# Performance work log

Measured on AMD Instinct MI355X. Metric: run time of the kernel, lower is better.

The kernel has to match this reference:

```python
import jax, jax.numpy as jnp
import numpy as np

B, N, F, FS, OUT, S, H, K = 1024, 256, 64, 128, 128, 4, 4, 4
EPS = 1e-5   # BatchNorm1d eps
BIG = 1e9    # sentinel distance for invalid nodes

# fully-connected segment edges (S nodes per graph, B graphs, flat node indexing)
_base = np.array([(i, j) for i in range(S) for j in range(S) if i != j], dtype=np.int32).T
_offs = (np.arange(B, dtype=np.int32) * S)[:, None]
CSRC = jnp.asarray((_base[0][None, :] + _offs).reshape(-1))
CDST = jnp.asarray((_base[1][None, :] + _offs).reshape(-1))
CMASK = jnp.ones(CSRC.shape[0], jnp.float32)


def _bn_relu(h, gamma, beta):
    # BatchNorm1d in training mode: biased batch statistics over the node axis
    mu = h.mean(0)
    var = jnp.var(h, axis=0)
    return jax.nn.relu((h - mu) * jax.lax.rsqrt(var + EPS) * gamma + beta)


def _graph_conv(x, src, dst, emask, W, b, gamma, beta):
    # linear -> gather(src) -> scatter-add(dst) -> degree norm -> BN -> ReLU
    h = x @ W + b
    agg = jax.ops.segment_sum(h[src] * emask[:, None], dst, num_segments=x.shape[0])
    deg = jnp.clip(jax.ops.segment_sum(emask, dst, num_segments=x.shape[0]), 1.0, None)
    return _bn_relu(h + agg / deg[:, None], gamma, beta)


def _knn_edges(positions, presence):
    # edges (i -> j) for each valid node i to its K nearest valid neighbors j
    valid = presence > 0.5                                    # [B,N]
    n_valid = valid.sum(-1)                                   # [B]
    diff = positions[:, :, None, :] - positions[:, None, :, :]
    d2 = jax.lax.stop_gradient(jnp.sum(diff * diff, -1))      # squared dist, same ordering as cdist
    d2 = jnp.where(valid[:, None, :], d2, BIG)                # mask invalid columns
    negv, idx = jax.lax.top_k(-d2, K + 1)                     # nearest first; idx[...,0] is self (dist 0)
    nbr, nd = idx[:, :, 1:], -negv[:, :, 1:]                  # [B,N,K]
    emask = valid[:, :, None] & (n_valid[:, None, None] >= 2) & (nd < 0.5 * BIG)
    offs = (jnp.arange(B) * N)[:, None, None]
    src = jnp.broadcast_to(jnp.arange(N)[None, :, None] + offs, (B, N, K)).reshape(-1)
    dst = jnp.where(emask, nbr + offs, 0).reshape(-1)
    return src, dst, emask.reshape(-1).astype(jnp.float32)


def setup_inputs() -> dict:
    key = jax.random.key(0)
    ks = jax.random.split(key, 16)
    rn = lambda k, shp, s=0.05: jax.random.normal(k, shp, jnp.float32) * s
    return {
        "axle_features": jax.random.normal(ks[0], (B, N, F), jnp.float32),
        "axle_positions": jax.random.normal(ks[1], (B, N, 2), jnp.float32),
        "presence_scores": jax.random.uniform(ks[2], (B, N), jnp.float32),
        "seg_queries": jax.random.normal(ks[3], (S, F), jnp.float32),
        "wq": rn(ks[4], (F, F)), "bq": jnp.zeros((F,), jnp.float32),
        "wk": rn(ks[5], (F, F)), "bk": jnp.zeros((F,), jnp.float32),
        "w_a2s": rn(ks[6], (F, FS)), "b_a2s": jnp.zeros((FS,), jnp.float32),
        "w_s2a": rn(ks[7], (FS, F)), "b_s2a": jnp.zeros((F,), jnp.float32),
        "coarse_W": rn(ks[8], (2, FS, FS)), "coarse_b": jnp.zeros((2, FS), jnp.float32),
        "coarse_gamma": jnp.ones((2, FS), jnp.float32), "coarse_beta": jnp.zeros((2, FS), jnp.float32),
        "fine_W": rn(ks[9], (3, F, F)), "fine_b": jnp.zeros((3, F), jnp.float32),
        "fine_gamma": jnp.ones((3, F), jnp.float32), "fine_beta": jnp.zeros((3, F), jnp.float32),
        "w_out": rn(ks[10], (F, OUT)), "b_out": jnp.zeros((OUT,), jnp.float32),
    }


def reference(axle_features, axle_positions, presence_scores, seg_queries, wq, bq, wk, bk,
              w_a2s, b_a2s, w_s2a, b_s2a, coarse_W, coarse_b, coarse_gamma, coarse_beta,
              fine_W, fine_b, fine_gamma, fine_beta, w_out, b_out):
    hd = F // H
    # LearnableSegmentation: MHA attention weights (head-averaged), then softmax over segments
    q = (seg_queries @ wq + bq).reshape(S, H, hd)
    k = (axle_features @ wk + bk).reshape(B, N, H, hd)
    scores = jnp.einsum('shd,bnhd->bhsn', q, k) / np.sqrt(hd)
    attn = jax.nn.softmax(scores, -1).mean(1)                 # [B,S,N]
    assign = jax.nn.softmax(jnp.swapaxes(attn, 1, 2), -1)     # [B,N,S]
    # segment pooling + coarse GNN over fully-connected segment graph
    proj = axle_features @ w_a2s + b_a2s                      # [B,N,FS]
    sf = jnp.einsum('bns,bnf->bsf', assign, proj).reshape(B * S, FS)
    for l in range(coarse_W.shape[0]):
        sf = _graph_conv(sf, CSRC, CDST, CMASK, coarse_W[l], coarse_b[l], coarse_gamma[l], coarse_beta[l])
    ctx = jnp.einsum('bns,bsf->bnf', assign, sf.reshape(B, S, FS)) @ w_s2a + b_s2a
    # fine GNN over kNN axle graph
    src, dst, em = _knn_edges(axle_positions, presence_scores)
    af = (axle_features + ctx).reshape(B * N, F)
    for l in range(fine_W.shape[0]):
        af = _graph_conv(af, src, dst, em, fine_W[l], fine_b[l], fine_gamma[l], fine_beta[l])
    # presence-weighted pooling + output projection
    pw = presence_scores[:, :, None]
    g = (af.reshape(B, N, F) * pw).sum(1) / jnp.clip(pw.sum(1), 1e-8, None)
    return g @ w_out + b_out
```

## Files before the change

### kernel.cpp

```cpp
#include <hip/hip_runtime.h>
#include <hip/hip_bf16.h>
#include <math.h>

#define BB   1024
#define NN   256
#define FF   64
#define FSS  128
#define OUTT 128
#define SS   4
#define HH   4
#define KK   4
#define HDD  16
#define EPSF 1e-5f
#define BIGF 1000000000.0f
#define ROWB 72
#define ROWA 68

typedef __attribute__((ext_vector_type(8))) short short8;
typedef __attribute__((ext_vector_type(4))) float f32x4;

static __device__ __forceinline__ unsigned short f2bf(float f) {
  union { float f; unsigned u; } x; x.f = f;
  unsigned u = x.u + 0x7fffu + ((x.u >> 16) & 1u);
  return (unsigned short)(u >> 16);
}
static __device__ __forceinline__ float bf2f(unsigned short h) {
  union { unsigned u; float f; } x; x.u = ((unsigned)h) << 16;
  return x.f;
}
static __device__ __forceinline__ float bflo(unsigned u) {
  union { unsigned u; float f; } x; x.u = u << 16; return x.f;
}
static __device__ __forceinline__ float bfhi(unsigned u) {
  union { unsigned u; float f; } x; x.u = u & 0xffff0000u; return x.f;
}
static __device__ __forceinline__ unsigned pack2(float a, float b) {
  return (unsigned)f2bf(a) | ((unsigned)f2bf(b) << 16);
}

__global__ __launch_bounds__(256) void k_prep(
    const float* __restrict__ sq, const float* __restrict__ wq, const float* __restrict__ bq,
    const float* __restrict__ wk, const float* __restrict__ bk,
    float* __restrict__ V_o, float* __restrict__ c_o)
{
  const int tid = threadIdx.x;
  __shared__ float sq_s[SS*FF];
  __shared__ float q_s[SS*FF];
  sq_s[tid] = sq[tid];
  __syncthreads();
  {
    int s = tid >> 6, f = tid & 63;
    float acc = bq[f];
    for (int c = 0; c < FF; ++c) acc += sq_s[s*FF+c] * wq[c*FF+f];
    q_s[s*FF+f] = acc;
  }
  __syncthreads();
  {
    int c = tid & 63, jb = (tid >> 6) * 4;
    for (int jj = 0; jj < 4; ++jj) {
      int j = jb + jj, h = j >> 2, s = j & 3;
      float acc = 0.f;
      for (int d = 0; d < HDD; ++d)
        acc += wk[c*FF + h*HDD + d] * q_s[s*FF + h*HDD + d];
      V_o[c*16 + j] = acc * 0.25f;
    }
  }
  if (tid < 16) {
    int h = tid >> 2, s = tid & 3;
    float acc = 0.f;
    for (int d = 0; d < HDD; ++d) acc += bk[h*HDD+d] * q_s[s*FF + h*HDD + d];
    c_o[tid] = acc * 0.25f;
  }
}

__global__ __launch_bounds__(256, 3) void k_attn_sf(
    const float* __restrict__ axle,
    const float* __restrict__ Vm, const float* __restrict__ cv,
    const float* __restrict__ w_a2s, const float* __restrict__ b_a2s,
    float* __restrict__ assign_o, float* __restrict__ sf_o)
{
  const int b = blockIdx.x, tid = threadIdx.x;
  const int wv = tid >> 6, ln = tid & 63;
  __shared__ __align__(16) unsigned short xb_a[NN*ROWA];
  __shared__ __align__(16) unsigned char u_buf[16*NN*2];
  __shared__ float mz_s[16][2];
  __hip_bfloat16* sc_s = (__hip_bfloat16*)u_buf;
  float (*as_s)[SS]    = (float (*)[SS])u_buf;
  float* t_s           = (float*)(u_buf + 4096);
  float* As_s          = (float*)(u_buf + 4096 + 1024);

  const float* afb = axle + (size_t)b*NN*FF;
  const float4* in4 = reinterpret_cast<const float4*>(afb);
  for (int i4 = tid; i4 < NN*FF/4; i4 += 256) {
    float4 v = in4[i4];
    int n = i4 >> 4, c4 = (i4 & 15) * 4;
    uint2 pk; pk.x = pack2(v.x, v.y); pk.y = pack2(v.z, v.w);
    *reinterpret_cast<uint2*>(&xb_a[n*ROWA + c4]) = pk;
  }
  __syncthreads();

  {
    float sc[16];
    #pragma unroll
    for (int j = 0; j < 16; ++j) sc[j] = cv[j];
    #pragma unroll
    for (int k = 0; k < 16; ++k) {
      uint2 pk = *reinterpret_cast<const uint2*>(&xb_a[tid*ROWA + 4*k]);
      float x0 = bflo(pk.x), x1 = bfhi(pk.x), x2 = bflo(pk.y), x3 = bfhi(pk.y);
      #pragma unroll
      for (int j = 0; j < 16; ++j) {
        float a = fmaf(x0, Vm[(4*k+0)*16+j], sc[j]);
        a = fmaf(x1, Vm[(4*k+1)*16+j], a);
        a = fmaf(x2, Vm[(4*k+2)*16+j], a);
        sc[j] = fmaf(x3, Vm[(4*k+3)*16+j], a);
      }
    }
    #pragma unroll
    for (int j = 0; j < 16; ++j) sc_s[j*NN + tid] = __float2bfloat16(sc[j]);
  }
  __syncthreads();

  for (int r = 0; r < 4; ++r) {
    int row = wv*4 + r;
    float v0 = __bfloat162float(sc_s[row*NN + ln]);
    float v1 = __bfloat162float(sc_s[row*NN + ln + 64]);
    float v2 = __bfloat162float(sc_s[row*NN + ln + 128]);
    float v3 = __bfloat162float(sc_s[row*NN + ln + 192]);
    float m = fmaxf(fmaxf(v0,v1), fmaxf(v2,v3));
    #pragma unroll
    for (int o = 32; o; o >>= 1) m = fmaxf(m, __shfl_xor(m, o));
    float z = __expf(v0-m) + __expf(v1-m) + __expf(v2-m) + __expf(v3-m);
    #pragma unroll
    for (int o = 32; o; o >>= 1) z += __shfl_xor(z, o);
    if (ln == 0) { mz_s[row][0] = m; mz_s[row][1] = 1.f/z; }
  }
  __syncthreads();

  float4 av;
  {
    float at0 = 0.f, at1 = 0.f, at2 = 0.f, at3 = 0.f;
    #pragma unroll
    for (int h = 0; h < HH; ++h) {
      at0 += __expf(__bfloat162float(sc_s[(h*4+0)*NN + tid]) - mz_s[h*4+0][0]) * mz_s[h*4+0][1];
      at1 += __expf(__bfloat162float(sc_s[(h*4+1)*NN + tid]) - mz_s[h*4+1][0]) * mz_s[h*4+1][1];
      at2 += __expf(__bfloat162float(sc_s[(h*4+2)*NN + tid]) - mz_s[h*4+2][0]) * mz_s[h*4+2][1];
      at3 += __expf(__bfloat162float(sc_s[(h*4+3)*NN + tid]) - mz_s[h*4+3][0]) * mz_s[h*4+3][1];
    }
    at0 *= 0.25f; at1 *= 0.25f; at2 *= 0.25f; at3 *= 0.25f;
    float m = fmaxf(fmaxf(at0,at1), fmaxf(at2,at3));
    float e0=__expf(at0-m), e1=__expf(at1-m), e2=__expf(at2-m), e3=__expf(at3-m);
    float zi = 1.f/(e0+e1+e2+e3);
    av = make_float4(e0*zi, e1*zi, e2*zi, e3*zi);
    reinterpret_cast<float4*>(assign_o)[(size_t)b*NN + tid] = av;
  }
  __syncthreads();
  *reinterpret_cast<float4*>(&as_s[tid][0]) = av;
  __syncthreads();

  {
    int s = wv, half = ln >> 5, c2 = ln & 31;
    float t0 = 0.f, t1 = 0.f, aa = 0.f;
    int n0 = half * 128;
    for (int n = n0; n < n0 + 128; ++n) {
      float a = as_s[n][s];
      unsigned pk = *reinterpret_cast<const unsigned*>(&xb_a[n*ROWA + 2*c2]);
      t0 = fmaf(a, bflo(pk), t0);
      t1 = fmaf(a, bfhi(pk), t1);
      aa += a;
    }
    t0 += __shfl_xor(t0, 32);
    t1 += __shfl_xor(t1, 32);
    aa += __shfl_xor(aa, 32);
    if (half == 0) {
      t_s[s*FF + 2*c2]     = t0;
      t_s[s*FF + 2*c2 + 1] = t1;
      if (c2 == 0) As_s[s] = aa;
    }
  }
  __syncthreads();

  for (int o = tid; o < SS*FSS; o += 256) {
    int s = o >> 7, f = o & 127;
    float acc = As_s[s] * b_a2s[f];
    for (int c = 0; c < FF; ++c) acc += t_s[s*FF + c] * w_a2s[c*FSS+f];
    sf_o[((size_t)b*SS+s)*FSS+f] = acc;
  }
}

__global__ __launch_bounds__(128) void k_coarse(
    const float* __restrict__ in, const float* __restrict__ W, const float* __restrict__ bias,
    const float* __restrict__ pmu, const float* __restrict__ prstd,
    const float* __restrict__ pgamma, const float* __restrict__ pbeta, int applyBN,
    float* __restrict__ out, float2* __restrict__ stp)
{
  const int b = blockIdx.x, f = threadIdx.x;
  __shared__ float x_s[SS][FSS];
  #pragma unroll
  for (int i = 0; i < SS; ++i) {
    float v = in[((size_t)b*SS+i)*FSS + f];
    if (applyBN) v = fmaxf((v - pmu[f])*prstd[f]*pgamma[f] + pbeta[f], 0.f);
    x_s[i][f] = v;
  }
  __syncthreads();
  float h0 = bias[f], h1 = h0, h2 = h0, h3 = h0;
  for (int c = 0; c < FSS; ++c) {
    float w = W[c*FSS+f];
    h0 += x_s[0][c]*w; h1 += x_s[1][c]*w; h2 += x_s[2][c]*w; h3 += x_s[3][c]*w;
  }
  float s4 = h0+h1+h2+h3;
  const float inv3 = 1.f/3.f;
  float o0 = h0 + (s4-h0)*inv3;
  float o1 = h1 + (s4-h1)*inv3;
  float o2 = h2 + (s4-h2)*inv3;
  float o3 = h3 + (s4-h3)*inv3;
  size_t ob = (size_t)b*SS*FSS + f;
  out[ob] = o0; out[ob+FSS] = o1; out[ob+2*FSS] = o2; out[ob+3*FSS] = o3;
  stp[(size_t)b*FSS + f] = make_float2(o0+o1+o2+o3, o0*o0+o1*o1+o2*o2+o3*o3);
}

__global__ __launch_bounds__(256) void k_bnstats(
    const float2* __restrict__ sp, float* __restrict__ mu, float* __restrict__ rstd,
    float invcnt, int F)
{
  const int f = blockIdx.x, tid = threadIdx.x;
  float a = 0.f, q = 0.f;
  for (int j = tid; j < BB; j += 256) {
    float2 v = sp[(size_t)j*F + f];
    a += v.x; q += v.y;
  }
  #pragma unroll
  for (int o = 32; o; o >>= 1) { a += __shfl_xor(a, o); q += __shfl_xor(q, o); }
  __shared__ float ra[4], rq[4];
  int wv = tid >> 6;
  if ((tid & 63) == 0) { ra[wv] = a; rq[wv] = q; }
  __syncthreads();
  if (tid == 0) {
    float s = ra[0]+ra[1]+ra[2]+ra[3], ss = rq[0]+rq[1]+rq[2]+rq[3];
    float m = s*invcnt; float v = ss*invcnt - m*m;
    mu[f] = m; rstd[f] = 1.f / sqrtf(v + EPSF);
  }
}

__global__ __launch_bounds__(512) void k_knn_ctx(
    const float* __restrict__ pos, const float* __restrict__ pres,
    const float* __restrict__ axle, const float* __restrict__ hc1,
    const float* __restrict__ mu, const float* __restrict__ rstd,
    const float* __restrict__ gamma, const float* __restrict__ beta,
    const float* __restrict__ assign_i,
    const float* __restrict__ w_s2a, const float* __restrict__ b_s2a,
    int* __restrict__ rev_go, int* __restrict__ offs_go,
    float* __restrict__ ivd_o, unsigned short* __restrict__ af_o)
{
  const int b = blockIdx.x, tid = threadIdx.x;
  const int ln = tid & 63, wv = tid >> 6;
  const int n = tid >> 1, half = tid & 1;
  __shared__ float2 pp[NN];
  __shared__ int vld[NN];
  __shared__ int wcnt[4];
  __shared__ int wsum[4];
  __shared__ int nbr_s[NN*KK];
  __shared__ int cnti[NN], scn[NN], cur[NN];
  __shared__ __align__(16) int rev_s[NN*KK];
  __shared__ float csf[SS][FSS];
  __shared__ float u_s[SS][FF];

  if (tid < NN) {
    float2 p = reinterpret_cast<const float2*>(pos)[(size_t)b*NN + tid];
    float pr = pres[(size_t)b*NN + tid];
    int v = pr > 0.5f ? 1 : 0;
    vld[tid] = v;
    pp[tid] = v ? p : make_float2(3.4e38f, 3.4e38f);
    cnti[tid] = 0; cur[tid] = 0;
    reinterpret_cast<int4*>(rev_s)[tid] = make_int4(0,0,0,0);
    int cnt = v;
    #pragma unroll
    for (int o = 32; o; o >>= 1) cnt += __shfl_xor(cnt, o);
    if (ln == 0) wcnt[wv] = cnt;
  }
  __syncthreads();
  const int nv = wcnt[0]+wcnt[1]+wcnt[2]+wcnt[3];

  float2 sp = pp[n];
  const float xi = sp.x, yi = sp.y;
  float b0=3.4e38f, b1=b0, b2=b0, b3=b0, b4=b0;
  int   j0=0, j1=0, j2=0, j3=0, j4=0;
  const int jb = half << 7;
  for (int j = jb; j < jb + 128; ++j) {
    float2 q = pp[j];
    float dx = __fsub_rn(xi, q.x);
    float dy = __fsub_rn(yi, q.y);
    float d2 = __fadd_rn(__fmul_rn(dx,dx), __fmul_rn(dy,dy));
    if (d2 < b4) {
      b4 = d2; j4 = j;
      if (b4 < b3) { float t=b3; b3=b4; b4=t; int ti=j3; j3=j4; j4=ti; }
      if (b3 < b2) { float t=b2; b2=b3; b3=t; int ti=j2; j2=j3; j3=ti; }
      if (b2 < b1) { float t=b1; b1=b2; b2=t; int ti=j1; j1=j2; j2=ti; }
      if (b1 < b0) { float t=b0; b0=b1; b1=t; int ti=j0; j0=j1; j1=ti; }
    }
  }
  float c0 = __shfl_xor(b0,1), c1 = __shfl_xor(b1,1), c2 = __shfl_xor(b2,1),
        c3 = __shfl_xor(b3,1), c4 = __shfl_xor(b4,1);
  int   k0 = __shfl_xor(j0,1), k1 = __shfl_xor(j1,1), k2 = __shfl_xor(j2,1),
        k3 = __shfl_xor(j3,1), k4 = __shfl_xor(j4,1);

  if (half == 0) {
#define MSTEP(OD, OJ) do { bool ta = (b0 <= c0); \
    OD = ta ? b0 : c0; OJ = ta ? j0 : k0; \
    b0 = ta ? b1 : b0; j0 = ta ? j1 : j0; \
    b1 = ta ? b2 : b1; j1 = ta ? j2 : j1; \
    b2 = ta ? b3 : b2; j2 = ta ? j3 : j2; \
    b3 = ta ? b4 : b3; j3 = ta ? j4 : j3; \
    b4 = ta ? 3.4e38f : b4; \
    c0 = ta ? c0 : c1; k0 = ta ? k0 : k1; \
    c1 = ta ? c1 : c2; k1 = ta ? k1 : k2; \
    c2 = ta ? c2 : c3; k2 = ta ? k2 : k3; \
    c3 = ta ? c3 : c4; k3 = ta ? k3 : k4; \
    c4 = ta ? c4 : 3.4e38f; } while(0)
    float m0d, dd1, dd2, dd3, dd4; int m0j, i1, i2, i3, i4;
    MSTEP(m0d, m0j);
    MSTEP(dd1, i1); MSTEP(dd2, i2); MSTEP(dd3, i3); MSTEP(dd4, i4);
#undef MSTEP
    (void)m0d; (void)m0j;
    bool okrow = (vld[n] != 0) && (nv >= 2);
    int e0 = (okrow && dd1 < 0.5f*BIGF) ? i1 : -1;
    int e1 = (okrow && dd2 < 0.5f*BIGF) ? i2 : -1;
    int e2 = (okrow && dd3 < 0.5f*BIGF) ? i3 : -1;
    int e3 = (okrow && dd4 < 0.5f*BIGF) ? i4 : -1;
    nbr_s[n*KK+0] = e0; nbr_s[n*KK+1] = e1;
    nbr_s[n*KK+2] = e2; nbr_s[n*KK+3] = e3;
    if (e0 >= 0) atomicAdd(&cnti[e0], 1);
    if (e1 >= 0) atomicAdd(&cnti[e1], 1);
    if (e2 >= 0) atomicAdd(&cnti[e2], 1);
    if (e3 >= 0) atomicAdd(&cnti[e3], 1);
  }
  __syncthreads();

  {
    int val = (tid < NN) ? cnti[tid] : 0;
    #pragma unroll
    for (int o = 1; o < 64; o <<= 1) {
      int t = __shfl_up(val, o);
      if (ln >= o) val += t;
    }
    if (tid < NN && ln == 63) wsum[wv] = val;
    __syncthreads();
    if (tid < NN) {
      int offs = 0;
      #pragma unroll
      for (int w = 0; w < 4; ++w) if (w < wv) offs += wsum[w];
      scn[tid] = val + offs;
    }
  }
  __syncthreads();

  if (tid < NN) {
    #pragma unroll
    for (int k = 0; k < KK; ++k) {
      int d = nbr_s[tid*KK+k];
      if (d >= 0) {
        int pp2 = atomicAdd(&cur[d], 1);
        rev_s[scn[d] - cnti[d] + pp2] = tid;
      }
    }
  }
  __syncthreads();

  if (tid < NN) {
    int start = scn[tid] - cnti[tid];
    offs_go[(size_t)b*(NN+1) + tid] = start;
    if (tid == NN-1) offs_go[(size_t)b*(NN+1) + NN] = scn[NN-1];
    int cnt = cnti[tid];
    float r = 1.f / fmaxf((float)cnt, 1.f);
    ivd_o[(size_t)b*NN + tid] = cnt > 0 ? -r : r;
    reinterpret_cast<int4*>(rev_go)[(size_t)b*NN + tid] =
        *reinterpret_cast<int4*>(&rev_s[tid*KK]);
  }

  {
    int s = tid >> 7, f = tid & 127;
    float v = hc1[((size_t)b*SS+s)*FSS + f];
    csf[s][f] = fmaxf((v - mu[f])*rstd[f]*gamma[f] + beta[f], 0.f);
  }
  __syncthreads();
  if (tid < 256) {
    int s = tid >> 6, f = tid & 63;
    float acc = 0.f;
    for (int c = 0; c < FSS; ++c) acc += csf[s][c] * w_s2a[c*FF+f];
    u_s[s][f] = acc;
  }
  __syncthreads();
  const size_t gb = (size_t)b*NN*FF;
  const float4* ax4 = reinterpret_cast<const float4*>(axle + gb);
  uint2* out2 = reinterpret_cast<uint2*>(af_o + gb);
  for (int i4 = tid; i4 < NN*FF/4; i4 += 512) {
    int nn2 = i4 >> 4, c4 = (i4 & 15) * 4;
    float4 ax = ax4[i4];
    float4 ag = reinterpret_cast<const float4*>(assign_i)[(size_t)b*NN + nn2];
    float o0 = ax.x + b_s2a[c4+0] + ag.x*u_s[0][c4+0] + ag.y*u_s[1][c4+0] + ag.z*u_s[2][c4+0] + ag.w*u_s[3][c4+0];
    float o1 = ax.y + b_s2a[c4+1] + ag.x*u_s[0][c4+1] + ag.y*u_s[1][c4+1] + ag.z*u_s[2][c4+1] + ag.w*u_s[3][c4+1];
    float o2 = ax.z + b_s2a[c4+2] + ag.x*u_s[0][c4+2] + ag.y*u_s[1][c4+2] + ag.z*u_s[2][c4+2] + ag.w*u_s[3][c4+2];
    float o3 = ax.w + b_s2a[c4+3] + ag.x*u_s[0][c4+3] + ag.y*u_s[1][c4+3] + ag.z*u_s[2][c4+3] + ag.w*u_s[3][c4+3];
    uint2 pk; pk.x = pack2(o0, o1); pk.y = pack2(o2, o3);
    out2[i4] = pk;
  }
}

__global__ __launch_bounds__(512, 4) void k_fine3(
    unsigned short* __restrict__ af,
    const float* __restrict__ W, const float* __restrict__ bias,
    const float* __restrict__ pmu, const float* __restrict__ prstd,
    const float* __restrict__ pgamma, const float* __restrict__ pbeta, int applyBN,
    const int* __restrict__ rev_g, const int* __restrict__ offs_g,
    const float* __restrict__ ivd_g,
    float2* __restrict__ stp)
{
  const int b = blockIdx.x, tid = threadIdx.x;
  const int wv = tid >> 6, ln = tid & 63;
  const int l15 = ln & 15, g = ln >> 4;
  __shared__ __align__(16) unsigned short xb[NN*ROWB];
  __shared__ __align__(16) unsigned short wt[FF*ROWB];
  __shared__ __align__(16) int rev_s[NN*KK];
  __shared__ unsigned short offs_s[NN+1];
  __shared__ float ivd_s[NN];
  __shared__ float scale_s[FF], shift_s[FF];
  float* red1 = (float*)rev_s;
  float* red2 = red1 + 8*FF;

  if (tid < FF) {
    if (applyBN) {
      float sc = prstd[tid]*pgamma[tid];
      scale_s[tid] = sc; shift_s[tid] = pbeta[tid] - pmu[tid]*sc;
    } else { scale_s[tid] = 1.f; shift_s[tid] = 0.f; }
  }
  for (int i = tid; i < NN*KK; i += 512) rev_s[i] = rev_g[(size_t)b*NN*KK + i];
  if (tid <= NN) offs_s[tid] = (unsigned short)offs_g[(size_t)b*(NN+1) + tid];
  if (tid < NN) ivd_s[tid] = ivd_g[(size_t)b*NN + tid];

  {
    const int c = tid >> 3, f0 = (tid & 7) * 8;
    float4 w0 = *reinterpret_cast<const float4*>(&W[c*FF + f0]);
    float4 w1 = *reinterpret_cast<const float4*>(&W[c*FF + f0 + 4]);
    wt[(f0+0)*ROWB + c] = f2bf(w0.x);
    wt[(f0+1)*ROWB + c] = f2bf(w0.y);
    wt[(f0+2)*ROWB + c] = f2bf(w0.z);
    wt[(f0+3)*ROWB + c] = f2bf(w0.w);
    wt[(f0+4)*ROWB + c] = f2bf(w1.x);
    wt[(f0+5)*ROWB + c] = f2bf(w1.y);
    wt[(f0+6)*ROWB + c] = f2bf(w1.z);
    wt[(f0+7)*ROWB + c] = f2bf(w1.w);
  }

  unsigned short* afb = af + (size_t)b*NN*FF;
  const uint4* in8 = reinterpret_cast<const uint4*>(afb);
  __syncthreads();

  for (int i8 = tid; i8 < NN*FF/8; i8 += 512) {
    uint4 raw = in8[i8];
    int n = i8 >> 3, c8 = (i8 & 7) * 8;
    float v0 = bflo(raw.x), v1 = bfhi(raw.x), v2 = bflo(raw.y), v3 = bfhi(raw.y);
    float v4 = bflo(raw.z), v5 = bfhi(raw.z), v6 = bflo(raw.w), v7 = bfhi(raw.w);
    v0 = v0*scale_s[c8+0] + shift_s[c8+0];
    v1 = v1*scale_s[c8+1] + shift_s[c8+1];
    v2 = v2*scale_s[c8+2] + shift_s[c8+2];
    v3 = v3*scale_s[c8+3] + shift_s[c8+3];
    v4 = v4*scale_s[c8+4] + shift_s[c8+4];
    v5 = v5*scale_s[c8+5] + shift_s[c8+5];
    v6 = v6*scale_s[c8+6] + shift_s[c8+6];
    v7 = v7*scale_s[c8+7] + shift_s[c8+7];
    if (applyBN) {
      v0=fmaxf(v0,0.f); v1=fmaxf(v1,0.f); v2=fmaxf(v2,0.f); v3=fmaxf(v3,0.f);
      v4=fmaxf(v4,0.f); v5=fmaxf(v5,0.f); v6=fmaxf(v6,0.f); v7=fmaxf(v7,0.f);
    }
    uint4 pk;
    pk.x = pack2(v0, v1); pk.y = pack2(v2, v3);
    pk.z = pack2(v4, v5); pk.w = pack2(v6, v7);
    *reinterpret_cast<uint4*>(&xb[n*ROWB + c8]) = pk;
  }
  __syncthreads();

  const int nb = wv << 5;
#define GATH(J) float y##J; { const int n_ = nb + (J); \
    const int s0_ = offs_s[n_]; const int s1_ = offs_s[n_+1]; \
    float sum_ = 0.f; \
    for (int i_ = s0_; i_ < s1_; ++i_) sum_ += bf2f(xb[rev_s[i_]*ROWB + ln]); \
    y##J = bf2f(xb[n_*ROWB + ln]) + fabsf(ivd_s[n_])*sum_; }
  GATH(0)  GATH(1)  GATH(2)  GATH(3)  GATH(4)  GATH(5)  GATH(6)  GATH(7)
  GATH(8)  GATH(9)  GATH(10) GATH(11) GATH(12) GATH(13) GATH(14) GATH(15)
  GATH(16) GATH(17) GATH(18) GATH(19) GATH(20) GATH(21) GATH(22) GATH(23)
  GATH(24) GATH(25) GATH(26) GATH(27) GATH(28) GATH(29) GATH(30) GATH(31)
#undef GATH
  __syncthreads();
#define WRB(J) xb[(nb + (J))*ROWB + ln] = f2bf(y##J);
  WRB(0)  WRB(1)  WRB(2)  WRB(3)  WRB(4)  WRB(5)  WRB(6)  WRB(7)
  WRB(8)  WRB(9)  WRB(10) WRB(11) WRB(12) WRB(13) WRB(14) WRB(15)
  WRB(16) WRB(17) WRB(18) WRB(19) WRB(20) WRB(21) WRB(22) WRB(23)
  WRB(24) WRB(25) WRB(26) WRB(27) WRB(28) WRB(29) WRB(30) WRB(31)
#undef WRB

  short8 areg[2][2], breg[4][2];
  #pragma unroll
  for (int rt2 = 0; rt2 < 2; ++rt2)
    #pragma unroll
    for (int ks = 0; ks < 2; ++ks)
      areg[rt2][ks] = *reinterpret_cast<const short8*>(
          &xb[((2*wv+rt2)*16 + l15)*ROWB + ks*32 + g*8]);
  #pragma unroll
  for (int ct = 0; ct < 4; ++ct)
    #pragma unroll
    for (int ks = 0; ks < 2; ++ks)
      breg[ct][ks] = *reinterpret_cast<const short8*>(
          &wt[(ct*16 + l15)*ROWB + ks*32 + g*8]);

  f32x4 acc[2][4];
  #pragma unroll
  for (int rt2 = 0; rt2 < 2; ++rt2)
    #pragma unroll
    for (int ct = 0; ct < 4; ++ct)
      acc[rt2][ct] = (f32x4){0.f, 0.f, 0.f, 0.f};
  #pragma unroll
  for (int rt2 = 0; rt2 < 2; ++rt2)
    #pragma unroll
    for (int ct = 0; ct < 4; ++ct)
      #pragma unroll
      for (int ks = 0; ks < 2; ++ks)
        acc[rt2][ct] = __builtin_amdgcn_mfma_f32_16x16x32_bf16(
            areg[rt2][ks], breg[ct][ks], acc[rt2][ct], 0, 0, 0);

  float bias_c[4];
  #pragma unroll
  for (int ct = 0; ct < 4; ++ct) bias_c[ct] = bias[ct*16 + l15];
  float ps[4] = {0.f,0.f,0.f,0.f}, pss[4] = {0.f,0.f,0.f,0.f};
  #pragma unroll
  for (int rt2 = 0; rt2 < 2; ++rt2) {
    #pragma unroll
    for (int i = 0; i < 4; ++i) {
      int row = (2*wv+rt2)*16 + g*4 + i;
      float bfr = ivd_s[row] < 0.f ? 2.f : 1.f;
      #pragma unroll
      for (int ct = 0; ct < 4; ++ct) {
        float o = acc[rt2][ct][i] + bfr*bias_c[ct];
        afb[row*FF + ct*16 + l15] = f2bf(o);
        ps[ct] += o; pss[ct] += o*o;
      }
    }
  }
  #pragma unroll
  for (int ct = 0; ct < 4; ++ct) {
    float p = ps[ct], q = pss[ct];
    p += __shfl_xor(p, 16); p += __shfl_xor(p, 32);
    q += __shfl_xor(q, 16); q += __shfl_xor(q, 32);
    if (g == 0) { red1[wv*FF + ct*16 + l15] = p; red2[wv*FF + ct*16 + l15] = q; }
  }
  __syncthreads();

  if (tid < FF) {
    float s = 0.f, ss = 0.f;
    #pragma unroll
    for (int w = 0; w < 8; ++w) { s += red1[w*FF + tid]; ss += red2[w*FF + tid]; }
    stp[(size_t)b*FF + tid] = make_float2(s, ss);
  }
}

__global__ __launch_bounds__(256) void k_pool(
    const unsigned short* __restrict__ af, const float* __restrict__ pres,
    const float* __restrict__ pmu, const float* __restrict__ prstd,
    const float* __restrict__ pgamma, const float* __restrict__ pbeta,
    const float* __restrict__ w_out, const float* __restrict__ b_out,
    float* __restrict__ out)
{
  const int b = blockIdx.x, tid = threadIdx.x;
  const int wv = tid >> 6, ln = tid & 63;
  __shared__ float pr_s2[NN];
  __shared__ float red[FF][9];
  __shared__ float g_s[FF];
  __shared__ float prsum_s[4];
  float pw = pres[(size_t)b*NN + tid];
  pr_s2[tid] = pw;
  float t = pw;
  #pragma unroll
  for (int o = 32; o; o >>= 1) t += __shfl_xor(t, o);
  if (ln == 0) prsum_s[wv] = t;
  __syncthreads();

  const int c2 = (tid & 31) * 2, jrow = tid >> 5;
  float sc0 = prstd[c2+0]*pgamma[c2+0], sh0 = pbeta[c2+0] - pmu[c2+0]*sc0;
  float sc1 = prstd[c2+1]*pgamma[c2+1], sh1 = pbeta[c2+1] - pmu[c2+1]*sc1;
  float s0 = 0.f, s1 = 0.f;
  const unsigned* af2 = reinterpret_cast<const unsigned*>(af + (size_t)b*NN*FF);
  for (int n = jrow; n < NN; n += 8) {
    unsigned pk = af2[n*(FF/2) + (tid & 31)];
    float p = pr_s2[n];
    s0 += fmaxf(bflo(pk)*sc0 + sh0, 0.f) * p;
    s1 += fmaxf(bfhi(pk)*sc1 + sh1, 0.f) * p;
  }
  red[c2+0][jrow] = s0;
  red[c2+1][jrow] = s1;
  __syncthreads();
  if (tid < FF) {
    float s = 0.f;
    #pragma unroll
    for (int j = 0; j < 8; ++j) s += red[tid][j];
    float den = fmaxf(prsum_s[0]+prsum_s[1]+prsum_s[2]+prsum_s[3], 1e-8f);
    g_s[tid] = s / den;
  }
  __syncthreads();
  if (tid < OUTT) {
    float acc = b_out[tid];
    for (int f = 0; f < FF; ++f) acc += g_s[f] * w_out[f*OUTT + tid];
    out[(size_t)b*OUTT + tid] = acc;
  }
}

extern "C" void kernel_launch(void* const* d_in, const int* in_sizes, int n_in,
                              void* d_out, int out_size, void* d_ws, size_t ws_size,
                              hipStream_t stream) {
  (void)in_sizes; (void)n_in; (void)out_size; (void)ws_size;
  const float* axle  = (const float*)d_in[0];
  const float* pos   = (const float*)d_in[1];
  const float* pres  = (const float*)d_in[2];
  const float* sq    = (const float*)d_in[3];
  const float* wq    = (const float*)d_in[4];
  const float* bq    = (const float*)d_in[5];
  const float* wk    = (const float*)d_in[6];
  const float* bk    = (const float*)d_in[7];
  const float* w_a2s = (const float*)d_in[8];
  const float* b_a2s = (const float*)d_in[9];
  const float* w_s2a = (const float*)d_in[10];
  const float* b_s2a = (const float*)d_in[11];
  const float* cW    = (const float*)d_in[12];
  const float* cb    = (const float*)d_in[13];
  const float* cg    = (const float*)d_in[14];
  const float* cbe   = (const float*)d_in[15];
  const float* fW    = (const float*)d_in[16];
  const float* fb    = (const float*)d_in[17];
  const float* fg    = (const float*)d_in[18];
  const float* fbe   = (const float*)d_in[19];
  const float* wout  = (const float*)d_in[20];
  const float* bout  = (const float*)d_in[21];
  float* out = (float*)d_out;

  char* base = (char*)d_ws;
  size_t off = 0;
  auto alloc = [&](size_t nbytes) -> void* {
    void* p = base + off; off += (nbytes + 255) & ~(size_t)255; return p;
  };
  unsigned short* af = (unsigned short*)alloc((size_t)BB*NN*FF*2);
  float* assign = (float*)alloc((size_t)BB*NN*SS*4);
  float* sf     = (float*)alloc((size_t)BB*SS*FSS*4);
  float* hc0    = (float*)alloc((size_t)BB*SS*FSS*4);
  float* hc1    = (float*)alloc((size_t)BB*SS*FSS*4);
  int*   rev    = (int*)  alloc((size_t)BB*NN*KK*4);
  int*   offs   = (int*)  alloc((size_t)BB*(NN+1)*4);
  float* ivd    = (float*)alloc((size_t)BB*NN*4);
  float2* stp   = (float2*)alloc((size_t)BB*FSS*8);
  float* mu0    = (float*)alloc(FSS*4);
  float* rs0    = (float*)alloc(FSS*4);
  float* mu1    = (float*)alloc(FSS*4);
  float* rs1    = (float*)alloc(FSS*4);
  float* muF    = (float*)alloc(FF*4);
  float* rsF    = (float*)alloc(FF*4);
  float* Vm     = (float*)alloc(FF*16*4);
  float* cv     = (float*)alloc(16*4);

  k_prep<<<1, 256, 0, stream>>>(sq, wq, bq, wk, bk, Vm, cv);
  k_attn_sf<<<BB, 256, 0, stream>>>(axle, Vm, cv, w_a2s, b_a2s, assign, sf);

  k_coarse<<<BB, 128, 0, stream>>>(sf,  cW,          cb,     mu0, rs0, cg, cbe, 0, hc0, stp);
  k_bnstats<<<FSS, 256, 0, stream>>>(stp, mu0, rs0, 1.f/((float)BB*SS), FSS);
  k_coarse<<<BB, 128, 0, stream>>>(hc0, cW+FSS*FSS,  cb+FSS, mu0, rs0, cg, cbe, 1, hc1, stp);
  k_bnstats<<<FSS, 256, 0, stream>>>(stp, mu1, rs1, 1.f/((float)BB*SS), FSS);

  k_knn_ctx<<<BB, 512, 0, stream>>>(pos, pres, axle, hc1, mu1, rs1, cg+FSS, cbe+FSS,
                                    assign, w_s2a, b_s2a, rev, offs, ivd, af);

  k_fine3<<<BB, 512, 0, stream>>>(af, fW,         fb,      muF, rsF, fg,    fbe,    0, rev, offs, ivd, stp);
  k_bnstats<<<FF, 256, 0, stream>>>(stp, muF, rsF, 1.f/((float)BB*NN), FF);
  k_fine3<<<BB, 512, 0, stream>>>(af, fW+FF*FF,   fb+FF,   muF, rsF, fg,    fbe,    1, rev, offs, ivd, stp);
  k_bnstats<<<FF, 256, 0, stream>>>(stp, muF, rsF, 1.f/((float)BB*NN), FF);
  k_fine3<<<BB, 512, 0, stream>>>(af, fW+2*FF*FF, fb+2*FF, muF, rsF, fg+FF, fbe+FF, 1, rev, offs, ivd, stp);
  k_bnstats<<<FF, 256, 0, stream>>>(stp, muF, rsF, 1.f/((float)BB*NN), FF);

  k_pool<<<BB, 256, 0, stream>>>(af, pres, muF, rsF, fg+2*FF, fbe+2*FF, wout, bout, out);
}
```

Measured before the change: 257.9 us.

## Fuse first fine GNN layer into kNN/context kernel

The first fine graph-conv layer (gather-aggregate, MFMA linear, bias, BN partial stats) now runs inside the kNN/context kernel. The context-added features stay in shared memory instead of being written out as bf16 and read back, and one kernel launch disappears. The fused kernel needs much more LDS and more registers, which may lower occupancy. The applyBN flag is dropped from the remaining fine kernel because it now always applies BN.

```diff
diff --git a/kernel.cpp b/kernel.cpp
--- a/kernel.cpp
+++ b/kernel.cpp
@@ -241,19 +241,22 @@
   }
 }
 
-__global__ __launch_bounds__(512) void k_knn_ctx(
+__global__ __launch_bounds__(512) void k_knn_ctx_f1(
     const float* __restrict__ pos, const float* __restrict__ pres,
     const float* __restrict__ axle, const float* __restrict__ hc1,
     const float* __restrict__ mu, const float* __restrict__ rstd,
     const float* __restrict__ gamma, const float* __restrict__ beta,
     const float* __restrict__ assign_i,
     const float* __restrict__ w_s2a, const float* __restrict__ b_s2a,
+    const float* __restrict__ W1, const float* __restrict__ bias1,
     int* __restrict__ rev_go, int* __restrict__ offs_go,
-    float* __restrict__ ivd_o, unsigned short* __restrict__ af_o)
+    float* __restrict__ ivd_o, unsigned short* __restrict__ af_o,
+    float2* __restrict__ stp)
 {
   const int b = blockIdx.x, tid = threadIdx.x;
   const int ln = tid & 63, wv = tid >> 6;
   const int n = tid >> 1, half = tid & 1;
+  const int l15 = ln & 15, g = ln >> 4;
   __shared__ float2 pp[NN];
   __shared__ int vld[NN];
   __shared__ int wcnt[4];
@@ -263,6 +266,26 @@
   __shared__ __align__(16) int rev_s[NN*KK];
   __shared__ float csf[SS][FSS];
   __shared__ float u_s[SS][FF];
+  __shared__ __align__(16) unsigned short xb[NN*ROWB];
+  __shared__ __align__(16) unsigned short wt[FF*ROWB];
+  __shared__ unsigned short offs_s[NN+1];
+  __shared__ float ivd_s[NN];
+  float* red1 = (float*)rev_s;
+  float* red2 = red1 + 8*FF;
+
+  {
+    const int c = tid >> 3, f0 = (tid & 7) * 8;
+    float4 w0 = *reinterpret_cast<const float4*>(&W1[c*FF + f0]);
+    float4 w1 = *reinterpret_cast<const float4*>(&W1[c*FF + f0 + 4]);
+    wt[(f0+0)*ROWB + c] = f2bf(w0.x);
+    wt[(f0+1)*ROWB + c] = f2bf(w0.y);
+    wt[(f0+2)*ROWB + c] = f2bf(w0.z);
+    wt[(f0+3)*ROWB + c] = f2bf(w0.w);
+    wt[(f0+4)*ROWB + c] = f2bf(w1.x);
+    wt[(f0+5)*ROWB + c] = f2bf(w1.y);
+    wt[(f0+6)*ROWB + c] = f2bf(w1.z);
+    wt[(f0+7)*ROWB + c] = f2bf(w1.w);
+  }
 
   if (tid < NN) {
     float2 p = reinterpret_cast<const float2*>(pos)[(size_t)b*NN + tid];
@@ -368,10 +391,16 @@
   if (tid < NN) {
     int start = scn[tid] - cnti[tid];
     offs_go[(size_t)b*(NN+1) + tid] = start;
-    if (tid == NN-1) offs_go[(size_t)b*(NN+1) + NN] = scn[NN-1];
+    offs_s[tid] = (unsigned short)start;
+    if (tid == NN-1) {
+      offs_go[(size_t)b*(NN+1) + NN] = scn[NN-1];
+      offs_s[NN] = (unsigned short)scn[NN-1];
+    }
     int cnt = cnti[tid];
     float r = 1.f / fmaxf((float)cnt, 1.f);
-    ivd_o[(size_t)b*NN + tid] = cnt > 0 ? -r : r;
+    float iv = cnt > 0 ? -r : r;
+    ivd_s[tid] = iv;
+    ivd_o[(size_t)b*NN + tid] = iv;
     reinterpret_cast<int4*>(rev_go)[(size_t)b*NN + tid] =
         *reinterpret_cast<int4*>(&rev_s[tid*KK]);
   }
@@ -390,18 +419,103 @@
   }
   __syncthreads();
   const size_t gb = (size_t)b*NN*FF;
-  const float4* ax4 = reinterpret_cast<const float4*>(axle + gb);
-  uint2* out2 = reinterpret_cast<uint2*>(af_o + gb);
-  for (int i4 = tid; i4 < NN*FF/4; i4 += 512) {
-    int nn2 = i4 >> 4, c4 = (i4 & 15) * 4;
-    float4 ax = ax4[i4];
-    float4 ag = reinterpret_cast<const float4*>(assign_i)[(size_t)b*NN + nn2];
-    float o0 = ax.x + b_s2a[c4+0] + ag.x*u_s[0][c4+0] + ag.y*u_s[1][c4+0] + ag.z*u_s[2][c4+0] + ag.w*u_s[3][c4+0];
-    float o1 = ax.y + b_s2a[c4+1] + ag.x*u_s[0][c4+1] + ag.y*u_s[1][c4+1] + ag.z*u_s[2][c4+1] + ag.w*u_s[3][c4+1];
-    float o2 = ax.z + b_s2a[c4+2] + ag.x*u_s[0][c4+2] + ag.y*u_s[1][c4+2] + ag.z*u_s[2][c4+2] + ag.w*u_s[3][c4+2];
-    float o3 = ax.w + b_s2a[c4+3] + ag.x*u_s[0][c4+3] + ag.y*u_s[1][c4+3] + ag.z*u_s[2][c4+3] + ag.w*u_s[3][c4+3];
-    uint2 pk; pk.x = pack2(o0, o1); pk.y = pack2(o2, o3);
-    out2[i4] = pk;
+  {
+    const float4* ax4 = reinterpret_cast<const float4*>(axle + gb);
+    for (int i4 = tid; i4 < NN*FF/4; i4 += 512) {
+      int nn2 = i4 >> 4, c4 = (i4 & 15) * 4;
+      float4 ax = ax4[i4];
+      float4 ag = reinterpret_cast<const float4*>(assign_i)[(size_t)b*NN + nn2];
+      float o0 = ax.x + b_s2a[c4+0] + ag.x*u_s[0][c4+0] + ag.y*u_s[1][c4+0] + ag.z*u_s[2][c4+0] + ag.w*u_s[3][c4+0];
+      float o1 = ax.y + b_s2a[c4+1] + ag.x*u_s[0][c4+1] + ag.y*u_s[1][c4+1] + ag.z*u_s[2][c4+1] + ag.w*u_s[3][c4+1];
+      float o2 = ax.z + b_s2a[c4+2] + ag.x*u_s[0][c4+2] + ag.y*u_s[1][c4+2] + ag.z*u_s[2][c4+2] + ag.w*u_s[3][c4+2];
+      float o3 = ax.w + b_s2a[c4+3] + ag.x*u_s[0][c4+3] + ag.y*u_s[1][c4+3] + ag.z*u_s[2][c4+3] + ag.w*u_s[3][c4+3];
+      uint2 pk; pk.x = pack2(o0, o1); pk.y = pack2(o2, o3);
+      *reinterpret_cast<uint2*>(&xb[nn2*ROWB + c4]) = pk;
+    }
+  }
+  __syncthreads();
+
+  const int nb = wv << 5;
+#define GATH(J) float y##J; { const int n_ = nb + (J); \
+    const int s0_ = offs_s[n_]; const int s1_ = offs_s[n_+1]; \
+    float sum_ = 0.f; \
+    for (int i_ = s0_; i_ < s1_; ++i_) sum_ += bf2f(xb[rev_s[i_]*ROWB + ln]); \
+    y##J = bf2f(xb[n_*ROWB + ln]) + fabsf(ivd_s[n_])*sum_; }
+  GATH(0)  GATH(1)  GATH(2)  GATH(3)  GATH(4)  GATH(5)  GATH(6)  GATH(7)
+  GATH(8)  GATH(9)  GATH(10) GATH(11) GATH(12) GATH(13) GATH(14) GATH(15)
+  GATH(16) GATH(17) GATH(18) GATH(19) GATH(20) GATH(21) GATH(22) GATH(23)
+  GATH(24) GATH(25) GATH(26) GATH(27) GATH(28) GATH(29) GATH(30) GATH(31)
+#undef GATH
+  __syncthreads();
+#define WRB(J) xb[(nb + (J))*ROWB + ln] = f2bf(y##J);
+  WRB(0)  WRB(1)  WRB(2)  WRB(3)  WRB(4)  WRB(5)  WRB(6)  WRB(7)
+  WRB(8)  WRB(9)  WRB(10) WRB(11) WRB(12) WRB(13) WRB(14) WRB(15)
+  WRB(16) WRB(17) WRB(18) WRB(19) WRB(20) WRB(21) WRB(22) WRB(23)
+  WRB(24) WRB(25) WRB(26) WRB(27) WRB(28) WRB(29) WRB(30) WRB(31)
+#undef WRB
+
+  short8 areg[2][2], breg[4][2];
+  #pragma unroll
+  for (int rt2 = 0; rt2 < 2; ++rt2)
+    #pragma unroll
+    for (int ks = 0; ks < 2; ++ks)
+      areg[rt2][ks] = *reinterpret_cast<const short8*>(
+          &xb[((2*wv+rt2)*16 + l15)*ROWB + ks*32 + g*8]);
+  #pragma unroll
+  for (int ct = 0; ct < 4; ++ct)
+    #pragma unroll
+    for (int ks = 0; ks < 2; ++ks)
+      breg[ct][ks] = *reinterpret_cast<const short8*>(
+          &wt[(ct*16 + l15)*ROWB + ks*32 + g*8]);
+
+  f32x4 acc[2][4];
+  #pragma unroll
+  for (int rt2 = 0; rt2 < 2; ++rt2)
+    #pragma unroll
+    for (int ct = 0; ct < 4; ++ct)
+      acc[rt2][ct] = (f32x4){0.f, 0.f, 0.f, 0.f};
+  #pragma unroll
+  for (int rt2 = 0; rt2 < 2; ++rt2)
+    #pragma unroll
+    for (int ct = 0; ct < 4; ++ct)
+      #pragma unroll
+      for (int ks = 0; ks < 2; ++ks)
+        acc[rt2][ct] = __builtin_amdgcn_mfma_f32_16x16x32_bf16(
+            areg[rt2][ks], breg[ct][ks], acc[rt2][ct], 0, 0, 0);
+
+  unsigned short* afb2 = af_o + gb;
+  float bias_c[4];
+  #pragma unroll
+  for (int ct = 0; ct < 4; ++ct) bias_c[ct] = bias1[ct*16 + l15];
+  float ps[4] = {0.f,0.f,0.f,0.f}, pss[4] = {0.f,0.f,0.f,0.f};
+  #pragma unroll
+  for (int rt2 = 0; rt2 < 2; ++rt2) {
+    #pragma unroll
+    for (int i = 0; i < 4; ++i) {
+      int row = (2*wv+rt2)*16 + g*4 + i;
+      float bfr = ivd_s[row] < 0.f ? 2.f : 1.f;
+      #pragma unroll
+      for (int ct = 0; ct < 4; ++ct) {
+        float o = acc[rt2][ct][i] + bfr*bias_c[ct];
+        afb2[row*FF + ct*16 + l15] = f2bf(o);
+        ps[ct] += o; pss[ct] += o*o;
+      }
+    }
+  }
+  #pragma unroll
+  for (int ct = 0; ct < 4; ++ct) {
+    float p = ps[ct], q = pss[ct];
+    p += __shfl_xor(p, 16); p += __shfl_xor(p, 32);
+    q += __shfl_xor(q, 16); q += __shfl_xor(q, 32);
+    if (g == 0) { red1[wv*FF + ct*16 + l15] = p; red2[wv*FF + ct*16 + l15] = q; }
+  }
+  __syncthreads();
+
+  if (tid < FF) {
+    float s = 0.f, ss = 0.f;
+    #pragma unroll
+    for (int w = 0; w < 8; ++w) { s += red1[w*FF + tid]; ss += red2[w*FF + tid]; }
+    stp[(size_t)b*FF + tid] = make_float2(s, ss);
   }
 }
 
@@ -409,7 +523,7 @@
     unsigned short* __restrict__ af,
     const float* __restrict__ W, const float* __restrict__ bias,
     const float* __restrict__ pmu, const float* __restrict__ prstd,
-    const float* __restrict__ pgamma, const float* __restrict__ pbeta, int applyBN,
+    const float* __restrict__ pgamma, const float* __restrict__ pbeta,
     const int* __restrict__ rev_g, const int* __restrict__ offs_g,
     const float* __restrict__ ivd_g,
     float2* __restrict__ stp)
@@ -427,10 +541,8 @@
   float* red2 = red1 + 8*FF;
 
   if (tid < FF) {
-    if (applyBN) {
-      float sc = prstd[tid]*pgamma[tid];
-      scale_s[tid] = sc; shift_s[tid] = pbeta[tid] - pmu[tid]*sc;
-    } else { scale_s[tid] = 1.f; shift_s[tid] = 0.f; }
+    float sc = prstd[tid]*pgamma[tid];
+    scale_s[tid] = sc; shift_s[tid] = pbeta[tid] - pmu[tid]*sc;
   }
   for (int i = tid; i < NN*KK; i += 512) rev_s[i] = rev_g[(size_t)b*NN*KK + i];
   if (tid <= NN) offs_s[tid] = (unsigned short)offs_g[(size_t)b*(NN+1) + tid];
@@ -459,18 +571,14 @@
     int n = i8 >> 3, c8 = (i8 & 7) * 8;
     float v0 = bflo(raw.x), v1 = bfhi(raw.x), v2 = bflo(raw.y), v3 = bfhi(raw.y);
     float v4 = bflo(raw.z), v5 = bfhi(raw.z), v6 = bflo(raw.w), v7 = bfhi(raw.w);
-    v0 = v0*scale_s[c8+0] + shift_s[c8+0];
-    v1 = v1*scale_s[c8+1] + shift_s[c8+1];
-    v2 = v2*scale_s[c8+2] + shift_s[c8+2];
-    v3 = v3*scale_s[c8+3] + shift_s[c8+3];
-    v4 = v4*scale_s[c8+4] + shift_s[c8+4];
-    v5 = v5*scale_s[c8+5] + shift_s[c8+5];
-    v6 = v6*scale_s[c8+6] + shift_s[c8+6];
-    v7 = v7*scale_s[c8+7] + shift_s[c8+7];
-    if (applyBN) {
-      v0=fmaxf(v0,0.f); v1=fmaxf(v1,0.f); v2=fmaxf(v2,0.f); v3=fmaxf(v3,0.f);
-      v4=fmaxf(v4,0.f); v5=fmaxf(v5,0.f); v6=fmaxf(v6,0.f); v7=fmaxf(v7,0.f);
-    }
+    v0 = fmaxf(v0*scale_s[c8+0] + shift_s[c8+0], 0.f);
+    v1 = fmaxf(v1*scale_s[c8+1] + shift_s[c8+1], 0.f);
+    v2 = fmaxf(v2*scale_s[c8+2] + shift_s[c8+2], 0.f);
+    v3 = fmaxf(v3*scale_s[c8+3] + shift_s[c8+3], 0.f);
+    v4 = fmaxf(v4*scale_s[c8+4] + shift_s[c8+4], 0.f);
+    v5 = fmaxf(v5*scale_s[c8+5] + shift_s[c8+5], 0.f);
+    v6 = fmaxf(v6*scale_s[c8+6] + shift_s[c8+6], 0.f);
+    v7 = fmaxf(v7*scale_s[c8+7] + shift_s[c8+7], 0.f);
     uint4 pk;
     pk.x = pack2(v0, v1); pk.y = pack2(v2, v3);
     pk.z = pack2(v4, v5); pk.w = pack2(v6, v7);
@@ -670,14 +778,14 @@
   k_coarse<<<BB, 128, 0, stream>>>(hc0, cW+FSS*FSS,  cb+FSS, mu0, rs0, cg, cbe, 1, hc1, stp);
   k_bnstats<<<FSS, 256, 0, stream>>>(stp, mu1, rs1, 1.f/((float)BB*SS), FSS);
 
-  k_knn_ctx<<<BB, 512, 0, stream>>>(pos, pres, axle, hc1, mu1, rs1, cg+FSS, cbe+FSS,
-                                    assign, w_s2a, b_s2a, rev, offs, ivd, af);
-
-  k_fine3<<<BB, 512, 0, stream>>>(af, fW,         fb,      muF, rsF, fg,    fbe,    0, rev, offs, ivd, stp);
+  k_knn_ctx_f1<<<BB, 512, 0, stream>>>(pos, pres, axle, hc1, mu1, rs1, cg+FSS, cbe+FSS,
+                                       assign, w_s2a, b_s2a, fW, fb,
+                                       rev, offs, ivd, af, stp);
   k_bnstats<<<FF, 256, 0, stream>>>(stp, muF, rsF, 1.f/((float)BB*NN), FF);
-  k_fine3<<<BB, 512, 0, stream>>>(af, fW+FF*FF,   fb+FF,   muF, rsF, fg,    fbe,    1, rev, offs, ivd, stp);
+
+  k_fine3<<<BB, 512, 0, stream>>>(af, fW+FF*FF,   fb+FF,   muF, rsF, fg,    fbe,    rev, offs, ivd, stp);
   k_bnstats<<<FF, 256, 0, stream>>>(stp, muF, rsF, 1.f/((float)BB*NN), FF);
-  k_fine3<<<BB, 512, 0, stream>>>(af, fW+2*FF*FF, fb+2*FF, muF, rsF, fg+FF, fbe+FF, 1, rev, offs, ivd, stp);
+  k_fine3<<<BB, 512, 0, stream>>>(af, fW+2*FF*FF, fb+2*FF, muF, rsF, fg+FF, fbe+FF, rev, offs, ivd, stp);
   k_bnstats<<<FF, 256, 0, stream>>>(stp, muF, rsF, 1.f/((float)BB*NN), FF);
 
   k_pool<<<BB, 256, 0, stream>>>(af, pres, muF, rsF, fg+2*FF, fbe+2*FF, wout, bout, out);
```

Result: slower. 307.9 us (+19.4%).
